# Kernel optimization log

Hardware: AMD Instinct MI355X
Metric: run time of the kernel (lower is better)

## Reference

```python
import jax, jax.numpy as jnp
import numpy as np
from jax import lax

LN_EPS = 1e-6  # flax LayerNorm default


def _layernorm(x, scale, bias):
    mu = jnp.mean(x, axis=-1, keepdims=True)
    var = jnp.mean(jnp.square(x - mu), axis=-1, keepdims=True)
    return (x - mu) * lax.rsqrt(var + LN_EPS) * scale + bias


def _lstm_layer(c0, h0, Wi, Wh, b, x):
    # x: [B, T, F]; carry c/h: [B, H]; gate order i, f, g, o (flax)
    def step(carry, xt):
        c, h = carry
        z = xt @ Wi + h @ Wh + b  # [B, 4H]
        i, f, g, o = jnp.split(z, 4, axis=-1)
        i = jax.nn.sigmoid(i); f = jax.nn.sigmoid(f)
        g = jnp.tanh(g); o = jax.nn.sigmoid(o)
        c = f * c + i * g
        h = o * jnp.tanh(c)
        return (c, h), h
    (cT, hT), hs = lax.scan(step, (c0, h0), jnp.swapaxes(x, 0, 1))
    return cT, hT, jnp.swapaxes(hs, 0, 1)  # hs: [B, T, H]


def setup_inputs() -> dict:
    key = jax.random.key(0)
    ks = jax.random.split(key, 16)
    B, T, F, H, P, A = 64, 128, 512, 1024, 1024, 32
    s = 0.05
    return {
        "x": jax.random.normal(ks[0], (B, T, F), jnp.float32),
        "c0": jnp.zeros((2, B, H), jnp.float32),
        "h0": jnp.zeros((2, B, H), jnp.float32),
        "W_pre": jax.random.normal(ks[1], (F, P), jnp.float32) * s,
        "b_pre": jnp.zeros((P,), jnp.float32),
        "ln_scale": jnp.ones((P,), jnp.float32),
        "ln_bias": jnp.zeros((P,), jnp.float32),
        "Wi0": jax.random.normal(ks[2], (P, 4 * H), jnp.float32) * s,
        "Wh0": jax.random.normal(ks[3], (H, 4 * H), jnp.float32) * s,
        "b0": jnp.zeros((4 * H,), jnp.float32),
        "Wi1": jax.random.normal(ks[4], (H, 4 * H), jnp.float32) * s,
        "Wh1": jax.random.normal(ks[5], (H, 4 * H), jnp.float32) * s,
        "b1": jnp.zeros((4 * H,), jnp.float32),
        "W_post": jax.random.normal(ks[6], (H, P), jnp.float32) * s,
        "b_post": jnp.zeros((P,), jnp.float32),
        "W_out": jax.random.normal(ks[7], (P, A), jnp.float32) * s,
        "b_out": jnp.zeros((A,), jnp.float32),
        "training": False,
    }


def reference(x, c0, h0, W_pre, b_pre, ln_scale, ln_bias,
              Wi0, Wh0, b0, Wi1, Wh1, b1,
              W_post, b_post, W_out, b_out, training):
    # preprocessing: Dense -> LayerNorm -> relu
    h = jax.nn.relu(_layernorm(x @ W_pre + b_pre, ln_scale, ln_bias))
    # two stacked LSTM layers scanned over time
    c1, h1, h = _lstm_layer(c0[0], h0[0], Wi0, Wh0, b0, h)
    c2, h2, h = _lstm_layer(c0[1], h0[1], Wi1, Wh1, b1, h)
    # postprocessing: Dense -> relu (dropout deterministic => identity)
    h = jax.nn.relu(h @ W_post + b_post)
    logits = h @ W_out + b_out  # [B, T, action_dim]
    new_carry = (jnp.stack([c1, c2]), jnp.stack([h1, h2]))
    return new_carry, logits
```

## Files before the change

### kernel.cpp

```cpp
#include <hip/hip_runtime.h>
#include <hip/hip_bf16.h>
#include <math.h>

typedef __attribute__((ext_vector_type(8))) short short8;
typedef __attribute__((ext_vector_type(4))) float f32x4;
typedef __attribute__((ext_vector_type(4))) unsigned u32x4;
typedef unsigned short u16;
typedef unsigned long long u64;

__device__ __forceinline__ u16 f2bf(float f) {
    union { float f; unsigned u; } v; v.f = f;
    unsigned r = v.u + 0x7fffu + ((v.u >> 16) & 1u);
    return (u16)(r >> 16);
}
__device__ __forceinline__ float bf2f(u16 b) {
    union { unsigned u; float f; } v; v.u = ((unsigned)b) << 16;
    return v.f;
}
__device__ __forceinline__ float fast_sigmoid(float x) {
    return __builtin_amdgcn_rcpf(1.f + __expf(-x));
}
__device__ __forceinline__ float fast_tanh(float x) {
    return 1.f - 2.f * __builtin_amdgcn_rcpf(1.f + __expf(2.f * x));
}
__device__ __forceinline__ u32x4 ldg16(const void* p) {
    u32x4 r;
    asm volatile("global_load_dwordx4 %0, %1, off"
                 : "=v"(r) : "v"(p) : "memory");
    return r;
}


__global__ __launch_bounds__(256) void k_zero(unsigned* p, int n) {
    int i = blockIdx.x * 256 + threadIdx.x;
    if (i < n) p[i] = 0u;
}

__global__ __launch_bounds__(256) void k_cvt(const float* __restrict__ in,
                                             u16* __restrict__ out, int n) {
    int i = blockIdx.x * 256 + threadIdx.x;
    if (i < n) out[i] = f2bf(in[i]);
}

__global__ __launch_bounds__(256) void k_cvt_h(const float* __restrict__ in,
                                               u16* __restrict__ out) {
    int i = blockIdx.x * 256 + threadIdx.x;
    int b = i >> 10, j = i & 1023;
    out[(size_t)(j >> 3) * 512 + b * 8 + (j & 7)] = f2bf(in[i]);
}

__global__ __launch_bounds__(256) void k_transpose(const float* __restrict__ W,
                                                   u16* __restrict__ WT, int K, int N) {
    __shared__ float tile[32][33];
    int n0 = blockIdx.x * 32, k0 = blockIdx.y * 32;
    int tx = threadIdx.x & 31, ty = threadIdx.x >> 5;
    #pragma unroll
    for (int j = 0; j < 32; j += 8)
        tile[ty + j][tx] = W[(size_t)(k0 + ty + j) * N + n0 + tx];
    __syncthreads();
    #pragma unroll
    for (int j = 0; j < 32; j += 8)
        WT[(size_t)(n0 + ty + j) * K + k0 + tx] = f2bf(tile[tx][ty + j]);
}

template <int MODE>
__global__ __launch_bounds__(256) void k_gemm(const u16* __restrict__ A,
                                              const u16* __restrict__ BT,
                                              const float* __restrict__ bias,
                                              void* __restrict__ Cout,
                                              int M, int N, int K) {
    const int w = threadIdx.x >> 6, l = threadIdx.x & 63;
    const int lm = l & 15, lq = l >> 4;
    const int r0 = blockIdx.y * 64 + w * 16;
    const int c0 = blockIdx.x * 64;
    const u16* arow = A + (size_t)(r0 + lm) * K + lq * 8;
    const u16* bp0 = BT + (size_t)(c0 + lm) * K + lq * 8;
    const u16* bp1 = bp0 + (size_t)16 * K;
    const u16* bp2 = bp0 + (size_t)32 * K;
    const u16* bp3 = bp0 + (size_t)48 * K;
    f32x4 acc0 = {0.f, 0.f, 0.f, 0.f}, acc1 = acc0, acc2 = acc0, acc3 = acc0;
    for (int k0 = 0; k0 < K; k0 += 32) {
        short8 a = *(const short8*)(arow + k0);
        acc0 = __builtin_amdgcn_mfma_f32_16x16x32_bf16(a, *(const short8*)(bp0 + k0), acc0, 0, 0, 0);
        acc1 = __builtin_amdgcn_mfma_f32_16x16x32_bf16(a, *(const short8*)(bp1 + k0), acc1, 0, 0, 0);
        acc2 = __builtin_amdgcn_mfma_f32_16x16x32_bf16(a, *(const short8*)(bp2 + k0), acc2, 0, 0, 0);
        acc3 = __builtin_amdgcn_mfma_f32_16x16x32_bf16(a, *(const short8*)(bp3 + k0), acc3, 0, 0, 0);
    }
    f32x4 accs[4] = {acc0, acc1, acc2, acc3};
    #pragma unroll
    for (int nt = 0; nt < 4; nt++) {
        #pragma unroll
        for (int r = 0; r < 4; r++) {
            int row = r0 + lq * 4 + r;
            int col = c0 + nt * 16 + lm;
            float v = accs[nt][r] + bias[col];
            if (MODE == 0) {
                ((float*)Cout)[(size_t)row * N + col] = v;
            } else {
                if (MODE == 2) v = fmaxf(v, 0.f);
                ((u16*)Cout)[(size_t)row * N + col] = f2bf(v);
            }
        }
    }
}

__global__ __launch_bounds__(256) void k_ln_relu(const float* __restrict__ X,
                                                 const float* __restrict__ scale,
                                                 const float* __restrict__ bias,
                                                 u16* __restrict__ preS) {
    const int N = 1024;
    int row = blockIdx.x;
    int b = row >> 7, t = row & 127;
    const float* x = X + (size_t)row * N;
    __shared__ float vbuf[1024];
    float s = 0.f, ss = 0.f;
    float vals[4];
    #pragma unroll
    for (int j = 0; j < 4; j++) {
        float v = x[threadIdx.x + 256 * j];
        vals[j] = v; s += v; ss += v * v;
    }
    #pragma unroll
    for (int o = 32; o > 0; o >>= 1) { s += __shfl_down(s, o); ss += __shfl_down(ss, o); }
    __shared__ float rs[4], rss[4];
    int w = threadIdx.x >> 6;
    if ((threadIdx.x & 63) == 0) { rs[w] = s; rss[w] = ss; }
    __syncthreads();
    __shared__ float smu, sinv;
    if (threadIdx.x == 0) {
        float a = rs[0] + rs[1] + rs[2] + rs[3];
        float bq = rss[0] + rss[1] + rss[2] + rss[3];
        float mu = a * (1.f / N);
        float var = bq * (1.f / N) - mu * mu;
        smu = mu; sinv = rsqrtf(var + 1e-6f);
    }
    __syncthreads();
    float mu = smu, inv = sinv;
    #pragma unroll
    for (int j = 0; j < 4; j++) {
        int i = threadIdx.x + 256 * j;
        float v = (vals[j] - mu) * inv * scale[i] + bias[i];
        vbuf[i] = fmaxf(v, 0.f);
    }
    __syncthreads();
    if (threadIdx.x < 128) {
        int g = threadIdx.x;
        union { u16 h[8]; u32x4 v; } pk;
        #pragma unroll
        for (int e = 0; e < 8; e++) pk.h[e] = f2bf(vbuf[g * 8 + e]);
        *(u32x4*)(preS + (size_t)t * 65536 + (size_t)g * 512 + b * 8) = pk.v;
    }
}

#define FBLOCKS 256
__global__ __launch_bounds__(512, 1) void k_lstm_fused(
    const u16* __restrict__ WiT0, const u16* __restrict__ WhT0,
    const u16* __restrict__ WiT1, const u16* __restrict__ WhT1,
    const u16* __restrict__ preS, const float* __restrict__ b0v,
    const float* __restrict__ b1v, const float* __restrict__ c0_all,
    u16* __restrict__ hs0, u16* __restrict__ hs1, u16* __restrict__ Hp,
    float* __restrict__ out, unsigned* __restrict__ ctr) {
    const int bk = blockIdx.x;
    const int role = bk >> 7;
    const int bkl = bk & 127;
    const int tid = threadIdx.x;
    const int w = tid >> 6, l = tid & 63, lm = l & 15, lq = l >> 4;
    const int kp = w >> 2, rt = w & 3;

    __shared__ u16 whs[65536];
    __shared__ float zbuf[2 * 64 * 33];

    {
        const u16* Wx = role ? WiT1 : WiT0;
        const u16* Wh = role ? WhT1 : WhT0;
        for (int f = tid; f < 8192; f += 512) {
            int flm = f & 15, flq = (f >> 4) & 3;
            int fi = (f >> 6) & 31;
            int rest = f >> 11;
            int fg = rest & 1, fkp = (rest >> 1) & 1;
            int lc = fg * 16 + flm;
            int gcolw = (lc >> 3) * 1024 + bkl * 8 + (lc & 7);
            int k = fi * 32 + flq * 8;
            const u16* src = (fkp == 0 ? Wx : Wh) + (size_t)gcolw * 1024 + k;
            *(short8*)(whs + (size_t)f * 8) = *(const short8*)src;
        }
    }
    const int u = tid & 7, b = tid >> 3;
    const int gcol = bkl * 8 + u;
    float c = (c0_all + (size_t)role * 65536)[(size_t)b * 1024 + gcol];
    const float* bv = role ? b1v : b0v;
    float bi0 = bv[gcol], bi1 = bv[1024 + gcol];
    float bi2 = bv[2048 + gcol], bi3 = bv[3072 + gcol];
    u16* hs_my = role ? hs1 : hs0;
    float* c_out = out + (size_t)role * 65536;
    float* h_out = out + 131072 + (size_t)role * 65536;
    const int lanoff = (lq * 16 + lm) * 8;
    __syncthreads();

    for (int t = 0; t < 128; t++) {
        {
            unsigned need = 0; int base = 0; int dowait = 0;
            if (!role) {
                if (kp == 1 && t > 0) { need = 16u * (unsigned)t; base = 0; dowait = 1; }
            } else {
                if (kp == 0)          { need = 16u * (unsigned)(t + 1); base = 0; dowait = 1; }
                else if (t > 0)       { need = 16u * (unsigned)t; base = 8; dowait = 1; }
            }
            if (dowait) {
                for (;;) {
                    unsigned v = need;
                    if (l < 8)
                        v = __hip_atomic_load(&ctr[(base + l) * 16], __ATOMIC_RELAXED,
                                              __HIP_MEMORY_SCOPE_AGENT);
                    if (__all((int)(v >= need))) break;
                    __builtin_amdgcn_s_sleep(1);
                }
            }
        }

        const u16* abase;
        if (!role) abase = (kp == 0) ? preS + (size_t)t * 65536
                                     : hs0 + (size_t)t * 65536;
        else       abase = (kp == 0) ? hs0 + (size_t)(t + 1) * 65536
                                     : hs1 + (size_t)t * 65536;
        const u16* arow = abase + (size_t)lq * 512 + (rt * 16 + lm) * 8;
        const u16* bw0 = whs + kp * 32768 + lanoff;

        f32x4 acc0 = {0.f, 0.f, 0.f, 0.f}, acc1 = acc0;
        #define STEPF(Ai, i)                                                      \
        {   union { u32x4 q; short8 v; } _a; _a.q = (Ai);                         \
            short8 _b0 = *(const short8*)(bw0 + (i) * 512);                       \
            short8 _b1 = *(const short8*)(bw0 + 16384 + (i) * 512);               \
            acc0 = __builtin_amdgcn_mfma_f32_16x16x32_bf16(_a.v, _b0, acc0, 0, 0, 0); \
            acc1 = __builtin_amdgcn_mfma_f32_16x16x32_bf16(_a.v, _b1, acc1, 0, 0, 0); }

        u32x4 A0 = ldg16(arow +     0), A1 = ldg16(arow +  2048);
        u32x4 A2 = ldg16(arow +  4096), A3 = ldg16(arow +  6144);
        u32x4 A4 = ldg16(arow +  8192), A5 = ldg16(arow + 10240);
        u32x4 A6 = ldg16(arow + 12288), A7 = ldg16(arow + 14336);
        u32x4 A8 = ldg16(arow + 16384), A9 = ldg16(arow + 18432);
        u32x4 A10 = ldg16(arow + 20480), A11 = ldg16(arow + 22528);
        u32x4 A12 = ldg16(arow + 24576), A13 = ldg16(arow + 26624);
        u32x4 A14 = ldg16(arow + 28672), A15 = ldg16(arow + 30720);
        u32x4 A16 = ldg16(arow + 32768), A17 = ldg16(arow + 34816);
        u32x4 A18 = ldg16(arow + 36864), A19 = ldg16(arow + 38912);
        u32x4 A20 = ldg16(arow + 40960), A21 = ldg16(arow + 43008);
        u32x4 A22 = ldg16(arow + 45056), A23 = ldg16(arow + 47104);
        u32x4 A24 = ldg16(arow + 49152), A25 = ldg16(arow + 51200);
        u32x4 A26 = ldg16(arow + 53248), A27 = ldg16(arow + 55296);
        u32x4 A28 = ldg16(arow + 57344), A29 = ldg16(arow + 59392);
        u32x4 A30 = ldg16(arow + 61440), A31 = ldg16(arow + 63488);
        __builtin_amdgcn_s_setprio(1);
        asm volatile("s_waitcnt vmcnt(24)"
                     : "+v"(A0), "+v"(A1), "+v"(A2), "+v"(A3),
                       "+v"(A4), "+v"(A5), "+v"(A6), "+v"(A7) :: "memory");
        STEPF(A0, 0) STEPF(A1, 1) STEPF(A2, 2) STEPF(A3, 3)
        STEPF(A4, 4) STEPF(A5, 5) STEPF(A6, 6) STEPF(A7, 7)
        asm volatile("s_waitcnt vmcnt(16)"
                     : "+v"(A8), "+v"(A9), "+v"(A10), "+v"(A11),
                       "+v"(A12), "+v"(A13), "+v"(A14), "+v"(A15) :: "memory");
        STEPF(A8, 8) STEPF(A9, 9) STEPF(A10, 10) STEPF(A11, 11)
        STEPF(A12, 12) STEPF(A13, 13) STEPF(A14, 14) STEPF(A15, 15)
        asm volatile("s_waitcnt vmcnt(8)"
                     : "+v"(A16), "+v"(A17), "+v"(A18), "+v"(A19),
                       "+v"(A20), "+v"(A21), "+v"(A22), "+v"(A23) :: "memory");
        STEPF(A16, 16) STEPF(A17, 17) STEPF(A18, 18) STEPF(A19, 19)
        STEPF(A20, 20) STEPF(A21, 21) STEPF(A22, 22) STEPF(A23, 23)
        asm volatile("s_waitcnt vmcnt(0)"
                     : "+v"(A24), "+v"(A25), "+v"(A26), "+v"(A27),
                       "+v"(A28), "+v"(A29), "+v"(A30), "+v"(A31) :: "memory");
        STEPF(A24, 24) STEPF(A25, 25) STEPF(A26, 26) STEPF(A27, 27)
        STEPF(A28, 28) STEPF(A29, 29) STEPF(A30, 30) STEPF(A31, 31)
        __builtin_amdgcn_s_setprio(0);
        #undef STEPF

        {
            float* zb = zbuf + (size_t)kp * 2112;
            #pragma unroll
            for (int r = 0; r < 4; r++) {
                int row = rt * 16 + lq * 4 + r;
                zb[row * 33 + lm] = acc0[r];
                zb[row * 33 + 16 + lm] = acc1[r];
            }
        }
        __syncthreads();

        {
            const float* z0 = zbuf + (size_t)b * 33;
            const float* z1 = z0 + 2112;
            float gi = z0[u]      + z1[u]      + bi0;
            float gf = z0[8 + u]  + z1[8 + u]  + bi1;
            float gg = z0[16 + u] + z1[16 + u] + bi2;
            float go = z0[24 + u] + z1[24 + u] + bi3;
            gi = fast_sigmoid(gi);
            gf = fast_sigmoid(gf);
            gg = fast_tanh(gg);
            go = fast_sigmoid(go);
            c = gf * c + gi * gg;
            float h = go * fast_tanh(c);
            unsigned hv = (unsigned)f2bf(h);
            int base = l & 56;
            unsigned p0 = __shfl(hv, base + 0, 64) | (__shfl(hv, base + 1, 64) << 16);
            unsigned p1 = __shfl(hv, base + 2, 64) | (__shfl(hv, base + 3, 64) << 16);
            unsigned p2 = __shfl(hv, base + 4, 64) | (__shfl(hv, base + 5, 64) << 16);
            unsigned p3 = __shfl(hv, base + 6, 64) | (__shfl(hv, base + 7, 64) << 16);
            if (u == 0) {
                u32x4 pv = {p0, p1, p2, p3};
                u16* dst = hs_my + (size_t)(t + 1) * 65536 + (size_t)bkl * 512 + b * 8;
                asm volatile("global_store_dwordx4 %0, %1, off sc0 sc1"
                             :: "v"(dst), "v"(pv) : "memory");
                if (role) {
                    u16* d2 = Hp + (size_t)(t * 64 + b) * 1024 + bkl * 8;
                    *(u32x4*)d2 = pv;
                }
            }
            if (t == 127) {
                c_out[(size_t)b * 1024 + gcol] = c;
                h_out[(size_t)b * 1024 + gcol] = h;
            }
        }
        __syncthreads();

        if (tid == 0)
            __hip_atomic_fetch_add(&ctr[(role * 8 + (bkl & 7)) * 16], 1u,
                                   __ATOMIC_RELAXED, __HIP_MEMORY_SCOPE_AGENT);
    }
}

__global__ __launch_bounds__(256) void k_logits(const u16* __restrict__ Pact,
                                                const u16* __restrict__ WoT,
                                                const float* __restrict__ bout,
                                                float* __restrict__ out) {
    int r = blockIdx.x * 8 + (threadIdx.x >> 5);
    int n = threadIdx.x & 31;
    const u16* a = Pact + (size_t)r * 1024;
    const u16* wv = WoT + (size_t)n * 1024;
    float s = 0.f;
    for (int k = 0; k < 1024; k += 8) {
        short8 av = *(const short8*)(a + k);
        short8 wvv = *(const short8*)(wv + k);
        #pragma unroll
        for (int j = 0; j < 8; j++)
            s += bf2f((u16)av[j]) * bf2f((u16)wvv[j]);
    }
    int t = r >> 6, b = r & 63;
    out[((size_t)b * 128 + t) * 32 + n] = s + bout[n];
}

extern "C" void kernel_launch(void* const* d_in, const int* in_sizes, int n_in,
                              void* d_out, int out_size, void* d_ws, size_t ws_size,
                              hipStream_t stream) {
    const float* x      = (const float*)d_in[0];
    const float* c0     = (const float*)d_in[1];
    const float* h0     = (const float*)d_in[2];
    const float* W_pre  = (const float*)d_in[3];
    const float* b_pre  = (const float*)d_in[4];
    const float* ln_s   = (const float*)d_in[5];
    const float* ln_b   = (const float*)d_in[6];
    const float* Wi0    = (const float*)d_in[7];
    const float* Wh0    = (const float*)d_in[8];
    const float* b0     = (const float*)d_in[9];
    const float* Wi1    = (const float*)d_in[10];
    const float* Wh1    = (const float*)d_in[11];
    const float* b1     = (const float*)d_in[12];
    const float* W_post = (const float*)d_in[13];
    const float* b_post = (const float*)d_in[14];
    const float* W_out  = (const float*)d_in[15];
    const float* b_out  = (const float*)d_in[16];
    float* out = (float*)d_out;

    char* ws = (char*)d_ws;
    size_t off = 0;
    auto alloc = [&](size_t bytes) {
        void* p = ws + off;
        off += (bytes + 255) & ~(size_t)255;
        return p;
    };
    u16* WTpre  = (u16*)alloc((size_t)1024 * 512 * 2);
    u16* WTi0   = (u16*)alloc((size_t)4096 * 1024 * 2);
    u16* WTh0   = (u16*)alloc((size_t)4096 * 1024 * 2);
    u16* WTi1   = (u16*)alloc((size_t)4096 * 1024 * 2);
    u16* WTh1   = (u16*)alloc((size_t)4096 * 1024 * 2);
    u16* WTpost = (u16*)alloc((size_t)1024 * 1024 * 2);
    u16* WTout  = (u16*)alloc((size_t)32 * 1024 * 2);
    u16* Xb     = (u16*)alloc((size_t)8192 * 512 * 2);
    u16* preS   = (u16*)alloc((size_t)128 * 65536 * 2);
    u16* hs0    = (u16*)alloc((size_t)129 * 65536 * 2);
    u16* hs1    = (u16*)alloc((size_t)129 * 65536 * 2);
    u16* postact= (u16*)alloc((size_t)8192 * 1024 * 2);
    unsigned* ctr = (unsigned*)alloc(32768);
    void* unionreg = alloc((size_t)8192 * 4096 * 2);
    float* pre_f32 = (float*)unionreg;
    u16* Hplain = (u16*)unionreg;

    k_zero<<<32, 256, 0, stream>>>(ctr, 8192);
    k_cvt<<<(8192 * 512) / 256, 256, 0, stream>>>(x, Xb, 8192 * 512);
    k_cvt_h<<<256, 256, 0, stream>>>(h0, hs0);
    k_cvt_h<<<256, 256, 0, stream>>>(h0 + 65536, hs1);

    k_transpose<<<dim3(32, 16), 256, 0, stream>>>(W_pre, WTpre, 512, 1024);
    k_transpose<<<dim3(128, 32), 256, 0, stream>>>(Wi0, WTi0, 1024, 4096);
    k_transpose<<<dim3(128, 32), 256, 0, stream>>>(Wh0, WTh0, 1024, 4096);
    k_transpose<<<dim3(128, 32), 256, 0, stream>>>(Wi1, WTi1, 1024, 4096);
    k_transpose<<<dim3(128, 32), 256, 0, stream>>>(Wh1, WTh1, 1024, 4096);
    k_transpose<<<dim3(32, 32), 256, 0, stream>>>(W_post, WTpost, 1024, 1024);
    k_transpose<<<dim3(1, 32), 256, 0, stream>>>(W_out, WTout, 1024, 32);

    k_gemm<0><<<dim3(16, 128), 256, 0, stream>>>(Xb, WTpre, b_pre, pre_f32, 8192, 1024, 512);
    k_ln_relu<<<8192, 256, 0, stream>>>(pre_f32, ln_s, ln_b, preS);

    {
        const u16* WiT0_ = WTi0; const u16* WhT0_ = WTh0;
        const u16* WiT1_ = WTi1; const u16* WhT1_ = WTh1;
        const u16* preS_ = preS; const float* b0_ = b0; const float* b1_ = b1;
        const float* c0_ = c0; u16* hs0_ = hs0; u16* hs1_ = hs1;
        u16* Hp_ = Hplain; float* out_ = out; unsigned* ctr_ = ctr;
        void* args[] = {&WiT0_, &WhT0_, &WiT1_, &WhT1_, &preS_, &b0_, &b1_,
                        &c0_, &hs0_, &hs1_, &Hp_, &out_, &ctr_};
        hipLaunchCooperativeKernel((void*)k_lstm_fused, dim3(FBLOCKS), dim3(512),
                                   args, 0, stream);
    }

    k_gemm<2><<<dim3(16, 128), 256, 0, stream>>>(Hplain, WTpost, b_post, postact,
                                                 8192, 1024, 1024);
    k_logits<<<1024, 256, 0, stream>>>(postact, WTout, b_out, out + 262144);
}
```

Measured before the change: 1.186 ms.

## Replace shared atomic counters with per-block flags and single-wave polling

Each block now publishes its progress by storing t+1 to its own flag slot, replacing atomic increments on eight shared counters. One wave per k-half polls all 128 producer flags and then releases its sibling waves through a workgroup-local shared flag, so the other waves stop hammering global memory. This cuts atomic contention and spin traffic in the per-timestep grid barrier. In exchange each poll reads 128 flags instead of 8 and adds an intra-block handoff. The s_setprio priority raise around the MFMA section is also dropped.

```diff
diff --git a/kernel.cpp b/kernel.cpp
--- a/kernel.cpp
+++ b/kernel.cpp
@@ -169,6 +169,7 @@
 
     __shared__ u16 whs[65536];
     __shared__ float zbuf[2 * 64 * 33];
+    __shared__ int gflag[2];
 
     {
         const u16* Wx = role ? WiT1 : WiT0;
@@ -185,6 +186,7 @@
             *(short8*)(whs + (size_t)f * 8) = *(const short8*)src;
         }
     }
+    if (tid == 0) { gflag[0] = -1; gflag[1] = -1; }
     const int u = tid & 7, b = tid >> 3;
     const int gcol = bkl * 8 + u;
     float c = (c0_all + (size_t)role * 65536)[(size_t)b * 1024 + gcol];
@@ -198,23 +200,26 @@
     __syncthreads();
 
     for (int t = 0; t < 128; t++) {
-        {
-            unsigned need = 0; int base = 0; int dowait = 0;
-            if (!role) {
-                if (kp == 1 && t > 0) { need = 16u * (unsigned)t; base = 0; dowait = 1; }
+        if (role || kp == 1) {
+            int need = (role && kp == 0) ? t + 1 : t;
+            if (rt == 0) {
+                if (need > 0) {
+                    int cbase = (role && kp) ? 128 : 0;
+                    for (;;) {
+                        unsigned a0 = __hip_atomic_load(&ctr[(cbase + l) * 16], __ATOMIC_RELAXED,
+                                                        __HIP_MEMORY_SCOPE_AGENT);
+                        unsigned a1 = __hip_atomic_load(&ctr[(cbase + 64 + l) * 16], __ATOMIC_RELAXED,
+                                                        __HIP_MEMORY_SCOPE_AGENT);
+                        if (__all((a0 >= (unsigned)need) && (a1 >= (unsigned)need))) break;
+                        __builtin_amdgcn_s_sleep(1);
+                    }
+                }
+                __hip_atomic_store(&gflag[kp], need, __ATOMIC_RELAXED,
+                                   __HIP_MEMORY_SCOPE_WORKGROUP);
             } else {
-                if (kp == 0)          { need = 16u * (unsigned)(t + 1); base = 0; dowait = 1; }
-                else if (t > 0)       { need = 16u * (unsigned)t; base = 8; dowait = 1; }
-            }
-            if (dowait) {
-                for (;;) {
-                    unsigned v = need;
-                    if (l < 8)
-                        v = __hip_atomic_load(&ctr[(base + l) * 16], __ATOMIC_RELAXED,
-                                              __HIP_MEMORY_SCOPE_AGENT);
-                    if (__all((int)(v >= need))) break;
+                while (__hip_atomic_load(&gflag[kp], __ATOMIC_RELAXED,
+                                         __HIP_MEMORY_SCOPE_WORKGROUP) < need)
                     __builtin_amdgcn_s_sleep(1);
-                }
             }
         }
 
@@ -250,7 +255,6 @@
         u32x4 A26 = ldg16(arow + 53248), A27 = ldg16(arow + 55296);
         u32x4 A28 = ldg16(arow + 57344), A29 = ldg16(arow + 59392);
         u32x4 A30 = ldg16(arow + 61440), A31 = ldg16(arow + 63488);
-        __builtin_amdgcn_s_setprio(1);
         asm volatile("s_waitcnt vmcnt(24)"
                      : "+v"(A0), "+v"(A1), "+v"(A2), "+v"(A3),
                        "+v"(A4), "+v"(A5), "+v"(A6), "+v"(A7) :: "memory");
@@ -271,7 +275,6 @@
                        "+v"(A28), "+v"(A29), "+v"(A30), "+v"(A31) :: "memory");
         STEPF(A24, 24) STEPF(A25, 25) STEPF(A26, 26) STEPF(A27, 27)
         STEPF(A28, 28) STEPF(A29, 29) STEPF(A30, 30) STEPF(A31, 31)
-        __builtin_amdgcn_s_setprio(0);
         #undef STEPF
 
         {
@@ -322,8 +325,8 @@
         __syncthreads();
 
         if (tid == 0)
-            __hip_atomic_fetch_add(&ctr[(role * 8 + (bkl & 7)) * 16], 1u,
-                                   __ATOMIC_RELAXED, __HIP_MEMORY_SCOPE_AGENT);
+            __hip_atomic_store(&ctr[bk * 16], (unsigned)(t + 1), __ATOMIC_RELAXED,
+                               __HIP_MEMORY_SCOPE_AGENT);
     }
 }
 
```

After: 1.154 ms. 1.03x faster.
